# Kernel optimization log

Measured on AMD Instinct MI355X. Metric: run time of the kernel, lower is better.

## Reference

```python
import jax, jax.numpy as jnp
import numpy as np

EPS = 1e-5
NEG_SLOPE = 0.01  # F.leaky_relu default

N0, N1, N2 = 100000, 25000, 5000
E0, E1 = 800000, 160000
D_IN, D_HID, D_OUT = 256, 256, 128


def setup_inputs() -> dict:
    key = jax.random.key(0)
    ks = jax.random.split(key, 16)
    inp = {
        "x": jax.random.normal(ks[0], (N0, D_IN), dtype=jnp.float32),
        "src0": jax.random.randint(ks[1], (E0,), 0, N0, dtype=jnp.int32),
        "dst0": jax.random.randint(ks[2], (E0,), 0, N1, dtype=jnp.int32),
        "val0": jnp.arange(E0, dtype=jnp.int32),
        "src1": jax.random.randint(ks[3], (E1,), 0, N1, dtype=jnp.int32),
        "dst1": jax.random.randint(ks[4], (E1,), 0, N2, dtype=jnp.int32),
        "val1": jnp.arange(E1, dtype=jnp.int32),
        "timestamps": jax.random.randint(ks[5], (E0 + E1,), 0, 100, dtype=jnp.int32),
        "time": 50,
        "interval": 10,
        # SAGEConv layer 1 (in -> hidden): lin_l (bias) on aggregated, lin_r (no bias) on root
        "W1l": jax.random.normal(ks[6], (D_IN, D_HID), dtype=jnp.float32) / np.sqrt(D_IN),
        "W1r": jax.random.normal(ks[7], (D_IN, D_HID), dtype=jnp.float32) / np.sqrt(D_IN),
        "b1": jnp.zeros((D_HID,), dtype=jnp.float32),
        # BatchNorm1d params (eval mode: running stats)
        "g1": jnp.ones((D_HID,), dtype=jnp.float32),
        "bt1": jnp.zeros((D_HID,), dtype=jnp.float32),
        "rm1": jax.random.normal(ks[8], (D_HID,), dtype=jnp.float32) * 0.1,
        "rv1": jax.random.uniform(ks[9], (D_HID,), dtype=jnp.float32) + 0.5,
        # SAGEConv layer 2 (hidden -> out)
        "W2l": jax.random.normal(ks[10], (D_HID, D_OUT), dtype=jnp.float32) / np.sqrt(D_HID),
        "W2r": jax.random.normal(ks[11], (D_HID, D_OUT), dtype=jnp.float32) / np.sqrt(D_HID),
        "b2": jnp.zeros((D_OUT,), dtype=jnp.float32),
    }
    return inp


def _time_mask(val, timestamps, time, interval):
    # time_sparse keeps edges whose timestamp is in {time, ..., time+interval-1}
    ts = timestamps[val]
    return (ts >= time) & (ts < time + interval)


def _sage_conv(x_src, x_tgt, src, dst, mask, Wl, Wr, b, n_tgt):
    m = mask.astype(x_src.dtype)
    msg = x_src[src] * m[:, None]               # [E, D] gather + mask
    agg = jax.ops.segment_sum(msg, dst, num_segments=n_tgt)
    deg = jax.ops.segment_sum(m, dst, num_segments=n_tgt)
    agg = agg / jnp.maximum(deg, 1.0)[:, None]  # mean aggregation
    return agg @ Wl + b + x_tgt @ Wr


def reference(x, src0, dst0, val0, src1, dst1, val1, timestamps, time, interval,
              W1l, W1r, b1, g1, bt1, rm1, rv1, W2l, W2r, b2):
    # layer 0: N0 -> N1
    mask0 = _time_mask(val0, timestamps, time, interval)
    h = _sage_conv(x, x[:N1], src0, dst0, mask0, W1l, W1r, b1, N1)
    # BatchNorm1d (eval) + leaky_relu; dropout is identity in eval
    h = (h - rm1) * jax.lax.rsqrt(rv1 + EPS) * g1 + bt1
    h = jnp.where(h >= 0, h, NEG_SLOPE * h)
    # layer 1: N1 -> N2
    mask1 = _time_mask(val1, timestamps, time, interval)
    out = _sage_conv(h, h[:N2], src1, dst1, mask1, W2l, W2r, b2, N2)
    return out, mask1
```

## Files before the change

kernel.cpp:

```cpp
#include <hip/hip_runtime.h>

#define N1c 25000
#define N2c 5000
#define Dc 256
#define DOUTc 128
#define EPSc 1e-5f
#define NEGc 0.01f

typedef __attribute__((ext_vector_type(8))) short short8;
typedef __attribute__((ext_vector_type(4))) float f32x4;

__device__ __forceinline__ ushort f2bf(float f) {
    unsigned u = __float_as_uint(f);
    u += 0x7fffu + ((u >> 16) & 1u);
    return (ushort)(u >> 16);
}
__device__ __forceinline__ float bf2f(ushort u) {
    return __uint_as_float(((unsigned)u) << 16);
}

__global__ __launch_bounds__(256) void prep_all(
    const float* __restrict__ x,
    const int* __restrict__ dst0, const int* __restrict__ val0,
    const int* __restrict__ dst1, const int* __restrict__ val1,
    const int* __restrict__ ts, const int* __restrict__ time_p, const int* __restrict__ itv_p,
    const float* __restrict__ W1l, const float* __restrict__ W1r,
    const float* __restrict__ W2l, const float* __restrict__ W2r,
    int E0, int E1,
    ushort* __restrict__ xb, ushort* __restrict__ Bt1, ushort* __restrict__ Bt2,
    int* __restrict__ count0, int* __restrict__ count1,
    float* __restrict__ mask_out) {
    const int flat = blockIdx.x * blockDim.x + threadIdx.x;
    const int NT = gridDim.x * blockDim.x;
    const int t0 = *time_p, iv = *itv_p;

    for (int i = flat; i < 256 * 512; i += NT) {
        int n = i >> 9, k = i & 511;
        float v = (k < 256) ? W1l[(size_t)k * 256 + n] : W1r[(size_t)(k - 256) * 256 + n];
        Bt1[i] = f2bf(v);
    }
    for (int i = flat; i < 128 * 512; i += NT) {
        int n = i >> 9, k = i & 511;
        float v = (k < 256) ? W2l[(size_t)k * 128 + n] : W2r[(size_t)(k - 256) * 128 + n];
        Bt2[i] = f2bf(v);
    }
    for (int e = flat; e < E1; e += NT) {
        int t = ts[val1[e]];
        mask_out[e] = (t >= t0 && t < t0 + iv) ? 1.0f : 0.0f;
    }
    for (int i = flat; i < N1c * 64; i += NT) {
        float4 v = ((const float4*)x)[i];
        ushort4 o;
        o.x = f2bf(v.x); o.y = f2bf(v.y); o.z = f2bf(v.z); o.w = f2bf(v.w);
        ((ushort4*)xb)[i] = o;
    }
    for (int e = flat; e < E0; e += NT) {
        int t = ts[val0[e]];
        if (t >= t0 && t < t0 + iv) atomicAdd(&count0[dst0[e]], 1);
    }
    for (int e = flat; e < E1; e += NT) {
        int t = ts[val1[e]];
        if (t >= t0 && t < t0 + iv) atomicAdd(&count1[dst1[e]], 1);
    }
}

template <int CH>
__device__ __forceinline__ void scan_block(const int* __restrict__ count,
                                           int* __restrict__ offsets, int n) {
    __shared__ int sums[1024];
    int t = threadIdx.x;
    int v[CH];
    int base = t * CH;
    int run = 0;
#pragma unroll
    for (int i = 0; i < CH; ++i) {
        int c = (base + i < n) ? count[base + i] : 0;
        v[i] = run;
        run += c;
    }
    sums[t] = run;
    __syncthreads();
    for (int off = 1; off < 1024; off <<= 1) {
        int s = (t >= off) ? sums[t - off] : 0;
        __syncthreads();
        sums[t] += s;
        __syncthreads();
    }
    int pre = t ? sums[t - 1] : 0;
#pragma unroll
    for (int i = 0; i < CH; ++i) {
        int idx = base + i;
        if (idx < n) offsets[idx] = pre + v[i];
    }
}

__global__ __launch_bounds__(1024) void scan_both(
    const int* __restrict__ count0, int* __restrict__ offsets0,
    const int* __restrict__ count1, int* __restrict__ offsets1) {
    if (blockIdx.x == 0) scan_block<25>(count0, offsets0, N1c);
    else                 scan_block<5>(count1, offsets1, N2c);
}

__global__ __launch_bounds__(256) void fill_both(
    const int* __restrict__ src0, const int* __restrict__ dst0, const int* __restrict__ val0,
    const int* __restrict__ src1, const int* __restrict__ dst1, const int* __restrict__ val1,
    const int* __restrict__ ts, const int* __restrict__ time_p, const int* __restrict__ itv_p,
    int E0, int E1,
    int* __restrict__ offsets0, int* __restrict__ offsets1,
    int* __restrict__ eidx0, int* __restrict__ eidx1) {
    int e = blockIdx.x * blockDim.x + threadIdx.x;
    int t0 = *time_p, iv = *itv_p;
    if (e < E0) {
        int t = ts[val0[e]];
        if (t >= t0 && t < t0 + iv) {
            int pos = atomicAdd(&offsets0[dst0[e]], 1);
            eidx0[pos] = src0[e];
        }
    } else if (e < E0 + E1) {
        int e1 = e - E0;
        int t = ts[val1[e1]];
        if (t >= t0 && t < t0 + iv) {
            int pos = atomicAdd(&offsets1[dst1[e1]], 1);
            eidx1[pos] = src1[e1];
        }
    }
}

__global__ void gather_f32(const float* __restrict__ X,
                           const int* __restrict__ off,
                           const int* __restrict__ eidx,
                           ushort* __restrict__ agg, int n) {
    int wave = (blockIdx.x * blockDim.x + threadIdx.x) >> 6;
    int lane = threadIdx.x & 63;
    if (wave >= n) return;
    int s1 = off[wave];
    int s0 = wave ? off[wave - 1] : 0;
    float4 acc = make_float4(0.f, 0.f, 0.f, 0.f);
    for (int j = s0; j < s1; ++j) {
        int s = eidx[j];
        float4 v = *(const float4*)(X + (size_t)s * Dc + lane * 4);
        acc.x += v.x; acc.y += v.y; acc.z += v.z; acc.w += v.w;
    }
    float inv = 1.0f / fmaxf((float)(s1 - s0), 1.0f);
    ushort4 o;
    o.x = f2bf(acc.x * inv); o.y = f2bf(acc.y * inv);
    o.z = f2bf(acc.z * inv); o.w = f2bf(acc.w * inv);
    *(ushort4*)(agg + (size_t)wave * Dc + lane * 4) = o;
}

__global__ void gather_bf16(const ushort* __restrict__ H,
                            const int* __restrict__ off,
                            const int* __restrict__ eidx,
                            ushort* __restrict__ agg, int n) {
    int wave = (blockIdx.x * blockDim.x + threadIdx.x) >> 6;
    int lane = threadIdx.x & 63;
    if (wave >= n) return;
    int s1 = off[wave];
    int s0 = wave ? off[wave - 1] : 0;
    float4 acc = make_float4(0.f, 0.f, 0.f, 0.f);
    for (int j = s0; j < s1; ++j) {
        int s = eidx[j];
        ushort4 v = *(const ushort4*)(H + (size_t)s * Dc + lane * 4);
        acc.x += bf2f(v.x); acc.y += bf2f(v.y);
        acc.z += bf2f(v.z); acc.w += bf2f(v.w);
    }
    float inv = 1.0f / fmaxf((float)(s1 - s0), 1.0f);
    ushort4 o;
    o.x = f2bf(acc.x * inv); o.y = f2bf(acc.y * inv);
    o.z = f2bf(acc.z * inv); o.w = f2bf(acc.w * inv);
    *(ushort4*)(agg + (size_t)wave * Dc + lane * 4) = o;
}

template <int VARIANT>
__global__ __launch_bounds__(128) void gemm_mfma(
    const ushort* __restrict__ Alo, const ushort* __restrict__ Ahi,
    const ushort* __restrict__ Bt,
    const float* __restrict__ bias,
    const float* __restrict__ g, const float* __restrict__ bt,
    const float* __restrict__ rm, const float* __restrict__ rv,
    void* __restrict__ Cout, int M) {
    __shared__ ushort As[64][40];
    __shared__ ushort Bs[128][40];
    int tid = threadIdx.x;
    int wave = tid >> 6, lane = tid & 63;
    int quad = lane >> 4, l16 = lane & 15;
    int m0 = blockIdx.y * 64, n0 = blockIdx.x * 128;
    f32x4 acc[2][8] = {};
    int ar = tid >> 1;
    int ak = (tid & 1) * 16;
    int bn = tid;
    for (int k0 = 0; k0 < 512; k0 += 32) {
        const ushort* Ag = (k0 < 256)
            ? (Alo + (size_t)(m0 + ar) * Dc + k0 + ak)
            : (Ahi + (size_t)(m0 + ar) * Dc + (k0 - 256) + ak);
        uint4 a0 = make_uint4(0, 0, 0, 0), a1 = make_uint4(0, 0, 0, 0);
        if (m0 + ar < M) {
            a0 = *(const uint4*)Ag;
            a1 = *(const uint4*)(Ag + 8);
        }
        const ushort* Bg = Bt + (size_t)(n0 + bn) * 512 + k0;
        uint4 b0 = *(const uint4*)(Bg + 0);
        uint4 b1 = *(const uint4*)(Bg + 8);
        uint4 b2 = *(const uint4*)(Bg + 16);
        uint4 b3 = *(const uint4*)(Bg + 24);
        __syncthreads();
        *(uint4*)&As[ar][ak] = a0;
        *(uint4*)&As[ar][ak + 8] = a1;
        *(uint4*)&Bs[bn][0] = b0;
        *(uint4*)&Bs[bn][8] = b1;
        *(uint4*)&Bs[bn][16] = b2;
        *(uint4*)&Bs[bn][24] = b3;
        __syncthreads();
        short8 af0 = *(const short8*)&As[wave * 32 + l16][quad * 8];
        short8 af1 = *(const short8*)&As[wave * 32 + 16 + l16][quad * 8];
#pragma unroll
        for (int j = 0; j < 8; ++j) {
            short8 bf = *(const short8*)&Bs[j * 16 + l16][quad * 8];
            acc[0][j] = __builtin_amdgcn_mfma_f32_16x16x32_bf16(af0, bf, acc[0][j], 0, 0, 0);
            acc[1][j] = __builtin_amdgcn_mfma_f32_16x16x32_bf16(af1, bf, acc[1][j], 0, 0, 0);
        }
    }
#pragma unroll
    for (int grp = 0; grp < 2; ++grp) {
#pragma unroll
        for (int j = 0; j < 8; ++j) {
            int gn = n0 + j * 16 + l16;
            float sc = 1.f, sh = bias[gn];
            if (VARIANT == 0) {
                float s = g[gn] * rsqrtf(rv[gn] + EPSc);
                sh = (bias[gn] - rm[gn]) * s + bt[gn];
                sc = s;
            }
            int gmb = m0 + wave * 32 + grp * 16 + quad * 4;
#pragma unroll
            for (int r = 0; r < 4; ++r) {
                int gm = gmb + r;
                if (gm >= M) continue;
                float v = acc[grp][j][r];
                if (VARIANT == 0) {
                    v = v * sc + sh;
                    v = v >= 0.f ? v : NEGc * v;
                    ((ushort*)Cout)[(size_t)gm * Dc + gn] = f2bf(v);
                } else {
                    ((float*)Cout)[(size_t)gm * DOUTc + gn] = v + sh;
                }
            }
        }
    }
}

extern "C" void kernel_launch(void* const* d_in, const int* in_sizes, int n_in,
                              void* d_out, int out_size, void* d_ws, size_t ws_size,
                              hipStream_t stream) {
    const float* x    = (const float*)d_in[0];
    const int* src0   = (const int*)d_in[1];
    const int* dst0   = (const int*)d_in[2];
    const int* val0   = (const int*)d_in[3];
    const int* src1   = (const int*)d_in[4];
    const int* dst1   = (const int*)d_in[5];
    const int* val1   = (const int*)d_in[6];
    const int* ts     = (const int*)d_in[7];
    const int* time_p = (const int*)d_in[8];
    const int* itv_p  = (const int*)d_in[9];
    const float* W1l  = (const float*)d_in[10];
    const float* W1r  = (const float*)d_in[11];
    const float* b1   = (const float*)d_in[12];
    const float* g1   = (const float*)d_in[13];
    const float* bt1  = (const float*)d_in[14];
    const float* rm1  = (const float*)d_in[15];
    const float* rv1  = (const float*)d_in[16];
    const float* W2l  = (const float*)d_in[17];
    const float* W2r  = (const float*)d_in[18];
    const float* b2   = (const float*)d_in[19];
    int E0 = in_sizes[1];
    int E1 = in_sizes[4];
    float* out = (float*)d_out;

    ushort* agg0 = (ushort*)d_ws;
    ushort* xb   = agg0 + (size_t)N1c * Dc;
    ushort* h    = xb   + (size_t)N1c * Dc;
    ushort* agg1 = h    + (size_t)N1c * Dc;
    ushort* Bt1  = agg1 + (size_t)N2c * Dc;
    ushort* Bt2  = Bt1  + 256 * 512;
    int* ip      = (int*)(Bt2 + 128 * 512);
    int* count0   = ip;            ip += N1c;
    int* count1   = ip;            ip += N2c;
    int* offsets0 = ip;            ip += N1c;
    int* offsets1 = ip;            ip += N2c;
    int* eidx0    = ip;            ip += E0;
    int* eidx1    = ip;            ip += E1;
    float* mask_tail = out + (size_t)N2c * DOUTc;

    hipMemsetAsync(count0, 0, (size_t)(N1c + N2c) * sizeof(int), stream);

    prep_all<<<1024, 256, 0, stream>>>(
        x, dst0, val0, dst1, val1, ts, time_p, itv_p,
        W1l, W1r, W2l, W2r, E0, E1, xb, Bt1, Bt2, count0, count1, mask_tail);
    scan_both<<<2, 1024, 0, stream>>>(count0, offsets0, count1, offsets1);
    fill_both<<<(E0 + E1 + 255) / 256, 256, 0, stream>>>(
        src0, dst0, val0, src1, dst1, val1, ts, time_p, itv_p,
        E0, E1, offsets0, offsets1, eidx0, eidx1);
    gather_f32<<<(N1c + 3) / 4, 256, 0, stream>>>(x, offsets0, eidx0, agg0, N1c);
    gemm_mfma<0><<<dim3(2, (N1c + 63) / 64), 128, 0, stream>>>(
        agg0, xb, Bt1, b1, g1, bt1, rm1, rv1, h, N1c);
    gather_bf16<<<(N2c + 3) / 4, 256, 0, stream>>>(h, offsets1, eidx1, agg1, N2c);
    gemm_mfma<1><<<dim3(1, (N2c + 63) / 64), 128, 0, stream>>>(
        agg1, h, Bt2, b2, nullptr, nullptr, nullptr, nullptr, out, N2c);
}
```

Baseline: 287.3 us.

## Fuse x bf16 conversion into GEMM, use shuffle scan, smaller second GEMM tile

The layer-1 GEMM now reads the fp32 root features directly and packs them to bf16 while loading tiles, so the separate conversion pass over x in prep_all goes away. The block scan is rewritten to use wave shuffles plus a 16-entry shared array in place of the log-step shared-memory loop with many barriers. The second GEMM uses a 32-row tile so more blocks cover the small N2 output. The trade-off is more fp32 bytes read per A tile inside the GEMM.

Measured after the change: 278.9 us. 3.0% less time.

```diff
diff --git a/kernel.cpp b/kernel.cpp
--- a/kernel.cpp
+++ b/kernel.cpp
@@ -18,16 +18,18 @@
 __device__ __forceinline__ float bf2f(ushort u) {
     return __uint_as_float(((unsigned)u) << 16);
 }
+__device__ __forceinline__ unsigned pack2(float lo, float hi) {
+    return ((unsigned)f2bf(lo)) | (((unsigned)f2bf(hi)) << 16);
+}
 
 __global__ __launch_bounds__(256) void prep_all(
-    const float* __restrict__ x,
     const int* __restrict__ dst0, const int* __restrict__ val0,
     const int* __restrict__ dst1, const int* __restrict__ val1,
     const int* __restrict__ ts, const int* __restrict__ time_p, const int* __restrict__ itv_p,
     const float* __restrict__ W1l, const float* __restrict__ W1r,
     const float* __restrict__ W2l, const float* __restrict__ W2r,
     int E0, int E1,
-    ushort* __restrict__ xb, ushort* __restrict__ Bt1, ushort* __restrict__ Bt2,
+    ushort* __restrict__ Bt1, ushort* __restrict__ Bt2,
     int* __restrict__ count0, int* __restrict__ count1,
     float* __restrict__ mask_out) {
     const int flat = blockIdx.x * blockDim.x + threadIdx.x;
@@ -48,12 +50,6 @@
         int t = ts[val1[e]];
         mask_out[e] = (t >= t0 && t < t0 + iv) ? 1.0f : 0.0f;
     }
-    for (int i = flat; i < N1c * 64; i += NT) {
-        float4 v = ((const float4*)x)[i];
-        ushort4 o;
-        o.x = f2bf(v.x); o.y = f2bf(v.y); o.z = f2bf(v.z); o.w = f2bf(v.w);
-        ((ushort4*)xb)[i] = o;
-    }
     for (int e = flat; e < E0; e += NT) {
         int t = ts[val0[e]];
         if (t >= t0 && t < t0 + iv) atomicAdd(&count0[dst0[e]], 1);
@@ -67,8 +63,9 @@
 template <int CH>
 __device__ __forceinline__ void scan_block(const int* __restrict__ count,
                                            int* __restrict__ offsets, int n) {
-    __shared__ int sums[1024];
+    __shared__ int wsum[16];
     int t = threadIdx.x;
+    int lane = t & 63, w = t >> 6;
     int v[CH];
     int base = t * CH;
     int run = 0;
@@ -78,15 +75,21 @@
         v[i] = run;
         run += c;
     }
-    sums[t] = run;
+    int incl = run;
+#pragma unroll
+    for (int off = 1; off < 64; off <<= 1) {
+        int s = __shfl_up(incl, off, 64);
+        if (lane >= off) incl += s;
+    }
+    if (lane == 63) wsum[w] = incl;
     __syncthreads();
-    for (int off = 1; off < 1024; off <<= 1) {
-        int s = (t >= off) ? sums[t - off] : 0;
-        __syncthreads();
-        sums[t] += s;
-        __syncthreads();
-    }
-    int pre = t ? sums[t - 1] : 0;
+    if (t == 0) {
+        int s = 0;
+#pragma unroll
+        for (int i = 0; i < 16; ++i) { int c = wsum[i]; wsum[i] = s; s += c; }
+    }
+    __syncthreads();
+    int pre = wsum[w] + (incl - run);
 #pragma unroll
     for (int i = 0; i < CH; ++i) {
         int idx = base + i;
@@ -171,32 +174,57 @@
     *(ushort4*)(agg + (size_t)wave * Dc + lane * 4) = o;
 }
 
-template <int VARIANT>
+template <int VARIANT, int GRPS>
 __global__ __launch_bounds__(128) void gemm_mfma(
-    const ushort* __restrict__ Alo, const ushort* __restrict__ Ahi,
+    const ushort* __restrict__ Alo,
+    const ushort* __restrict__ A2b, const float* __restrict__ A2f,
     const ushort* __restrict__ Bt,
     const float* __restrict__ bias,
     const float* __restrict__ g, const float* __restrict__ bt,
     const float* __restrict__ rm, const float* __restrict__ rv,
     void* __restrict__ Cout, int M) {
-    __shared__ ushort As[64][40];
+    constexpr int BM = 32 * GRPS;
+    constexpr int TPR = 128 / BM;
+    constexpr int CHUNK = 32 / TPR;
+    __shared__ ushort As[BM][40];
     __shared__ ushort Bs[128][40];
     int tid = threadIdx.x;
     int wave = tid >> 6, lane = tid & 63;
     int quad = lane >> 4, l16 = lane & 15;
-    int m0 = blockIdx.y * 64, n0 = blockIdx.x * 128;
-    f32x4 acc[2][8] = {};
-    int ar = tid >> 1;
-    int ak = (tid & 1) * 16;
+    int m0 = blockIdx.y * BM, n0 = blockIdx.x * 128;
+    f32x4 acc[GRPS][8] = {};
+    int ar = tid / TPR;
+    int ak = (tid % TPR) * CHUNK;
     int bn = tid;
     for (int k0 = 0; k0 < 512; k0 += 32) {
-        const ushort* Ag = (k0 < 256)
-            ? (Alo + (size_t)(m0 + ar) * Dc + k0 + ak)
-            : (Ahi + (size_t)(m0 + ar) * Dc + (k0 - 256) + ak);
         uint4 a0 = make_uint4(0, 0, 0, 0), a1 = make_uint4(0, 0, 0, 0);
-        if (m0 + ar < M) {
-            a0 = *(const uint4*)Ag;
-            a1 = *(const uint4*)(Ag + 8);
+        bool inb = (m0 + ar) < M;
+        if (k0 < 256) {
+            if (inb) {
+                const ushort* Ag = Alo + (size_t)(m0 + ar) * Dc + k0 + ak;
+                a0 = *(const uint4*)Ag;
+                if (CHUNK == 16) a1 = *(const uint4*)(Ag + 8);
+            }
+        } else if (VARIANT == 0) {
+            if (inb) {
+                const float* Af = A2f + (size_t)(m0 + ar) * Dc + (k0 - 256) + ak;
+                float4 f0 = *(const float4*)(Af + 0);
+                float4 f1 = *(const float4*)(Af + 4);
+                a0 = make_uint4(pack2(f0.x, f0.y), pack2(f0.z, f0.w),
+                                pack2(f1.x, f1.y), pack2(f1.z, f1.w));
+                if (CHUNK == 16) {
+                    float4 f2 = *(const float4*)(Af + 8);
+                    float4 f3 = *(const float4*)(Af + 12);
+                    a1 = make_uint4(pack2(f2.x, f2.y), pack2(f2.z, f2.w),
+                                    pack2(f3.x, f3.y), pack2(f3.z, f3.w));
+                }
+            }
+        } else {
+            if (inb) {
+                const ushort* Ag = A2b + (size_t)(m0 + ar) * Dc + (k0 - 256) + ak;
+                a0 = *(const uint4*)Ag;
+                if (CHUNK == 16) a1 = *(const uint4*)(Ag + 8);
+            }
         }
         const ushort* Bg = Bt + (size_t)(n0 + bn) * 512 + k0;
         uint4 b0 = *(const uint4*)(Bg + 0);
@@ -205,23 +233,26 @@
         uint4 b3 = *(const uint4*)(Bg + 24);
         __syncthreads();
         *(uint4*)&As[ar][ak] = a0;
-        *(uint4*)&As[ar][ak + 8] = a1;
+        if (CHUNK == 16) *(uint4*)&As[ar][ak + 8] = a1;
         *(uint4*)&Bs[bn][0] = b0;
         *(uint4*)&Bs[bn][8] = b1;
         *(uint4*)&Bs[bn][16] = b2;
         *(uint4*)&Bs[bn][24] = b3;
         __syncthreads();
-        short8 af0 = *(const short8*)&As[wave * 32 + l16][quad * 8];
-        short8 af1 = *(const short8*)&As[wave * 32 + 16 + l16][quad * 8];
+        short8 af[GRPS];
+#pragma unroll
+        for (int grp = 0; grp < GRPS; ++grp)
+            af[grp] = *(const short8*)&As[wave * 16 * GRPS + grp * 16 + l16][quad * 8];
 #pragma unroll
         for (int j = 0; j < 8; ++j) {
             short8 bf = *(const short8*)&Bs[j * 16 + l16][quad * 8];
-            acc[0][j] = __builtin_amdgcn_mfma_f32_16x16x32_bf16(af0, bf, acc[0][j], 0, 0, 0);
-            acc[1][j] = __builtin_amdgcn_mfma_f32_16x16x32_bf16(af1, bf, acc[1][j], 0, 0, 0);
-        }
-    }
-#pragma unroll
-    for (int grp = 0; grp < 2; ++grp) {
+#pragma unroll
+            for (int grp = 0; grp < GRPS; ++grp)
+                acc[grp][j] = __builtin_amdgcn_mfma_f32_16x16x32_bf16(af[grp], bf, acc[grp][j], 0, 0, 0);
+        }
+    }
+#pragma unroll
+    for (int grp = 0; grp < GRPS; ++grp) {
 #pragma unroll
         for (int j = 0; j < 8; ++j) {
             int gn = n0 + j * 16 + l16;
@@ -231,7 +262,7 @@
                 sh = (bias[gn] - rm[gn]) * s + bt[gn];
                 sc = s;
             }
-            int gmb = m0 + wave * 32 + grp * 16 + quad * 4;
+            int gmb = m0 + wave * 16 * GRPS + grp * 16 + quad * 4;
 #pragma unroll
             for (int r = 0; r < 4; ++r) {
                 int gm = gmb + r;
@@ -277,8 +308,7 @@
     float* out = (float*)d_out;
 
     ushort* agg0 = (ushort*)d_ws;
-    ushort* xb   = agg0 + (size_t)N1c * Dc;
-    ushort* h    = xb   + (size_t)N1c * Dc;
+    ushort* h    = agg0 + (size_t)N1c * Dc;
     ushort* agg1 = h    + (size_t)N1c * Dc;
     ushort* Bt1  = agg1 + (size_t)N2c * Dc;
     ushort* Bt2  = Bt1  + 256 * 512;
@@ -294,16 +324,16 @@
     hipMemsetAsync(count0, 0, (size_t)(N1c + N2c) * sizeof(int), stream);
 
     prep_all<<<1024, 256, 0, stream>>>(
-        x, dst0, val0, dst1, val1, ts, time_p, itv_p,
-        W1l, W1r, W2l, W2r, E0, E1, xb, Bt1, Bt2, count0, count1, mask_tail);
+        dst0, val0, dst1, val1, ts, time_p, itv_p,
+        W1l, W1r, W2l, W2r, E0, E1, Bt1, Bt2, count0, count1, mask_tail);
     scan_both<<<2, 1024, 0, stream>>>(count0, offsets0, count1, offsets1);
     fill_both<<<(E0 + E1 + 255) / 256, 256, 0, stream>>>(
         src0, dst0, val0, src1, dst1, val1, ts, time_p, itv_p,
         E0, E1, offsets0, offsets1, eidx0, eidx1);
     gather_f32<<<(N1c + 3) / 4, 256, 0, stream>>>(x, offsets0, eidx0, agg0, N1c);
-    gemm_mfma<0><<<dim3(2, (N1c + 63) / 64), 128, 0, stream>>>(
-        agg0, xb, Bt1, b1, g1, bt1, rm1, rv1, h, N1c);
+    gemm_mfma<0, 2><<<dim3(2, (N1c + 63) / 64), 128, 0, stream>>>(
+        agg0, nullptr, x, Bt1, b1, g1, bt1, rm1, rv1, h, N1c);
     gather_bf16<<<(N2c + 3) / 4, 256, 0, stream>>>(h, offsets1, eidx1, agg1, N2c);
-    gemm_mfma<1><<<dim3(1, (N2c + 63) / 64), 128, 0, stream>>>(
-        agg1, h, Bt2, b2, nullptr, nullptr, nullptr, nullptr, out, N2c);
-}
+    gemm_mfma<1, 1><<<dim3(1, (N2c + 31) / 32), 128, 0, stream>>>(
+        agg1, h, nullptr, Bt2, b2, nullptr, nullptr, nullptr, nullptr, out, N2c);
+}
```
